# Performance work log

Measured on AMD Instinct MI355X. Metric: run time of the kernel, lower is better.

## Reference

```python
import jax, jax.numpy as jnp
import numpy as np

B, N, F, E, K, R, H = 16, 2048, 2048, 128, 10, 2, 2


def setup_inputs() -> dict:
    key = jax.random.key(0)
    ks = jax.random.split(key, 11)
    s = 0.1  # keep embeddings close so the Gaussian kernel does not underflow
    rel = jax.random.normal(ks[0], (B, E), jnp.float32) * s
    arg1 = jax.random.normal(ks[1], (B, E), jnp.float32) * s
    arg2 = jax.random.normal(ks[2], (B, E), jnp.float32) * s
    fact_rel = jax.random.normal(ks[3], (B, F, E), jnp.float32) * s
    fact_arg1 = jax.random.normal(ks[4], (B, F, E), jnp.float32) * s
    fact_arg2 = jax.random.normal(ks[5], (B, F, E), jnp.float32) * s
    entity_embeddings = jax.random.normal(ks[6], (B, N, E), jnp.float32) * s
    hop_W = jax.random.normal(ks[7], (R, H, E, E), jnp.float32) / jnp.sqrt(jnp.float32(E))
    hop_b = jax.random.normal(ks[8], (R, H, E), jnp.float32) * 0.01
    nb_facts = jax.random.randint(ks[9], (B,), F // 2, F + 1, jnp.int32)
    nb_entities = jax.random.randint(ks[10], (B,), N // 2, N + 1, jnp.int32)
    return dict(rel=rel, arg1=arg1, arg2=arg2, fact_rel=fact_rel,
                fact_arg1=fact_arg1, fact_arg2=fact_arg2,
                entity_embeddings=entity_embeddings, hop_W=hop_W, hop_b=hop_b,
                nb_facts=nb_facts, nb_entities=nb_entities)


def reference(rel, arg1, arg2, fact_rel, fact_arg1, fact_arg2,
              entity_embeddings, hop_W, hop_b, nb_facts, nb_entities):
    # Gaussian kernel k(x,y) = exp(-||x-y||^2 / 2), batched: x [B,T,E], y [B,F,E] -> [B,T,F]
    def kern(x, y):
        d2 = (jnp.sum(x * x, -1)[:, :, None] + jnp.sum(y * y, -1)[:, None, :]
              - 2.0 * jnp.einsum('bte,bfe->btf', x, y))
        return jnp.exp(-0.5 * d2)

    fact_mask = (jnp.arange(F) < nb_facts[:, None])[:, None, :]            # [B,1,F]
    ent_mask = (jnp.arange(N) < nb_entities[:, None]).astype(rel.dtype)    # [B,N]

    # BatchNeuralKB.score: max over (valid) facts of product of kernels. [B,T,E]x3 -> [B,T]
    def model_score(r, a1, a2):
        s = kern(r, fact_rel) * kern(a1, fact_arg1) * kern(a2, fact_arg2)  # [B,T,F]
        return jnp.max(jnp.where(fact_mask, s, 0.0), axis=-1)

    # BatchNeuralKB.forward, (s,p,?) -> score per candidate object entity. [B,1,E] -> [B,N]
    def forward_sp(r, a1):
        kr = jnp.where(fact_mask, kern(r, fact_rel) * kern(a1, fact_arg1), 0.0)  # [B,1,F]
        kE = kern(entity_embeddings, fact_arg2)                                  # [B,N,F]
        return jnp.max(kr * kE, axis=-1) * ent_mask                              # [B,N]

    # (?,p,o) -> score per candidate subject entity
    def forward_po(r, a2):
        kr = jnp.where(fact_mask, kern(r, fact_rel) * kern(a2, fact_arg2), 0.0)
        kE = kern(entity_embeddings, fact_arg1)
        return jnp.max(kr * kE, axis=-1) * ent_mask

    # r_score(depth=1) = max(depth_r_score(0), depth_r_score(1))
    # depth_r_score(0) == model.score
    scores_0 = model_score(rel[:, None], arg1[:, None], arg2[:, None])[:, 0]  # [B]

    global_res = None
    for r_idx in range(R):
        is_rev = (r_idx % 2 == 1)
        # LinearReformulator: hop relations from rel
        h1 = rel @ hop_W[r_idx, 0] + hop_b[r_idx, 0]  # [B,E]
        h2 = rel @ hop_W[r_idx, 1] + hop_b[r_idx, 1]
        # hop 1: r_hop -> scores over all entities, then top-k beam
        if is_rev:
            sp = forward_po(h1[:, None], arg1[:, None])  # [B,N]
        else:
            sp = forward_sp(h1[:, None], arg1[:, None])
        z_scores, z_idx = jax.lax.top_k(sp, K)                                  # [B,K]
        z_emb = jnp.take_along_axis(entity_embeddings, z_idx[:, :, None], axis=1)  # [B,K,E]
        # final hop: r_score(depth=0) == model.score with branched args
        h2k = jnp.broadcast_to(h2[:, None, :], (B, K, E))
        a2k = jnp.broadcast_to(arg2[:, None, :], (B, K, E))
        if is_rev:
            s2 = model_score(h2k, a2k, z_emb)  # [B,K]
        else:
            s2 = model_score(h2k, z_emb, a2k)
        rule_scores = jnp.minimum(s2, z_scores)   # tnorm = 'min'
        rule_res = jnp.max(rule_scores, axis=1)   # max over branches [B]
        global_res = rule_res if global_res is None else jnp.maximum(global_res, rule_res)

    return jnp.maximum(scores_0, global_res)
```

## Files before the change

### kernel.cpp

```cpp
#include <hip/hip_runtime.h>
#include <math.h>

#define Bb 16
#define Nn 2048
#define Ff 2048
#define Ee 128
#define Kk 10
#define S2FC 8
#define S2F (Ff / S2FC)

typedef __attribute__((ext_vector_type(8))) short short8;
typedef __attribute__((ext_vector_type(4))) float f32x4;

__device__ inline float wave_sum(float x) {
    for (int o = 32; o; o >>= 1) x += __shfl_down(x, o);
    return x;
}

__device__ inline void bsplit(float x, unsigned short& h, unsigned short& l) {
    unsigned int u = __float_as_uint(x);
    h = (unsigned short)(u >> 16);
    float hf = __uint_as_float(u & 0xFFFF0000u);
    l = (unsigned short)(__float_as_uint(x - hf) >> 16);
}

__global__ __launch_bounds__(256) void k_bsplit(
    const float* __restrict__ fa1, const float* __restrict__ fa2,
    unsigned short* __restrict__ B0, unsigned short* __restrict__ B1) {
    int tid = threadIdx.x;
    int oct = tid & 15, fl = tid >> 4;
    int bx = blockIdx.x;
    int b = bx >> 7, f = (bx & 127) * 16 + fl;
    const float* src = (blockIdx.y == 0) ? fa2 : fa1;
    unsigned short* dst = ((blockIdx.y == 0) ? B0 : B1) +
                          (((size_t)b * 16 + oct) * Ff + f) * 16;
    const float* s = src + ((size_t)b * Ff + f) * Ee + oct * 8;
    float4 v0 = *(const float4*)s;
    float4 v1 = *(const float4*)(s + 4);
    float xs[8] = {v0.x, v0.y, v0.z, v0.w, v1.x, v1.y, v1.z, v1.w};
    unsigned short hi[8], lo[8];
#pragma unroll
    for (int j = 0; j < 8; ++j) bsplit(xs[j], hi[j], lo[j]);
    uint4 ph, pl;
    ph.x = (unsigned)hi[0] | ((unsigned)hi[1] << 16);
    ph.y = (unsigned)hi[2] | ((unsigned)hi[3] << 16);
    ph.z = (unsigned)hi[4] | ((unsigned)hi[5] << 16);
    ph.w = (unsigned)hi[6] | ((unsigned)hi[7] << 16);
    pl.x = (unsigned)lo[0] | ((unsigned)lo[1] << 16);
    pl.y = (unsigned)lo[2] | ((unsigned)lo[3] << 16);
    pl.z = (unsigned)lo[4] | ((unsigned)lo[5] << 16);
    pl.w = (unsigned)lo[6] | ((unsigned)lo[7] << 16);
    *(uint4*)dst = ph;
    *(uint4*)(dst + 8) = pl;
}

__global__ void k_hops(const float* __restrict__ rel, const float* __restrict__ hop_W,
                       const float* __restrict__ hop_b, float* __restrict__ h) {
    int rj = blockIdx.x;
    int b  = blockIdx.y;
    int e  = threadIdx.x;
    const float* W  = hop_W + (size_t)rj * Ee * Ee;
    const float* rb = rel + b * Ee;
    float acc = hop_b[rj * Ee + e];
    for (int i = 0; i < Ee; ++i) acc += rb[i] * W[i * Ee + e];
    h[((size_t)rj * Bb + b) * Ee + e] = acc;
}

__global__ void k_entnorm(const float* __restrict__ ent, float* __restrict__ ent_norm) {
    int row  = blockIdx.x * 4 + (threadIdx.x >> 6);
    int lane = threadIdx.x & 63;
    const float* p = ent + (size_t)row * Ee;
    float a = p[lane], c = p[lane + 64];
    float s = wave_sum(a * a + c * c);
    if (lane == 0) ent_norm[row] = s;
}

__global__ void k_facts(const float* __restrict__ rel, const float* __restrict__ arg1,
                        const float* __restrict__ arg2, const float* __restrict__ frel,
                        const float* __restrict__ fa1, const float* __restrict__ fa2,
                        const float* __restrict__ h, const int* __restrict__ nb_facts,
                        float* __restrict__ c0, float* __restrict__ c1,
                        float* __restrict__ s2b0, float* __restrict__ s2b1,
                        float* __restrict__ lsc0) {
    int f = blockIdx.x, b = blockIdx.y;
    int lane = threadIdx.x;
    size_t fb = ((size_t)b * Ff + f) * Ee;
    float d_rr = 0, d_a11 = 0, d_a22 = 0, d_h10 = 0, d_h11 = 0, d_h20 = 0, d_h21 = 0;
    float d_a12 = 0, d_a21 = 0, n1 = 0, n2 = 0;
#pragma unroll
    for (int half = 0; half < 2; ++half) {
        int e = lane + half * 64;
        float vr = frel[fb + e], v1 = fa1[fb + e], v2 = fa2[fb + e];
        float qr = rel[b * Ee + e], q1 = arg1[b * Ee + e], q2 = arg2[b * Ee + e];
        float h10 = h[((size_t)0 * Bb + b) * Ee + e];
        float h20 = h[((size_t)1 * Bb + b) * Ee + e];
        float h11 = h[((size_t)2 * Bb + b) * Ee + e];
        float h21 = h[((size_t)3 * Bb + b) * Ee + e];
        float t;
        t = qr - vr;  d_rr  += t * t;
        t = q1 - v1;  d_a11 += t * t;
        t = q2 - v2;  d_a22 += t * t;
        t = h10 - vr; d_h10 += t * t;
        t = h11 - vr; d_h11 += t * t;
        t = h20 - vr; d_h20 += t * t;
        t = h21 - vr; d_h21 += t * t;
        t = q1 - v2;  d_a12 += t * t;
        t = q2 - v1;  d_a21 += t * t;
        n1 += v1 * v1; n2 += v2 * v2;
    }
    d_rr = wave_sum(d_rr);   d_a11 = wave_sum(d_a11); d_a22 = wave_sum(d_a22);
    d_h10 = wave_sum(d_h10); d_h11 = wave_sum(d_h11); d_h20 = wave_sum(d_h20);
    d_h21 = wave_sum(d_h21); d_a12 = wave_sum(d_a12); d_a21 = wave_sum(d_a21);
    n1 = wave_sum(n1);       n2 = wave_sum(n2);
    if (lane == 0) {
        bool valid = f < nb_facts[b];
        const float NI = -INFINITY;
        size_t o = (size_t)b * Ff + f;
        lsc0[o] = valid ? -0.5f * (d_rr + d_a11 + d_a22) : NI;
        c0[o]   = valid ? (-0.5f * (d_h10 + d_a11 + n2)) : NI;
        c1[o]   = valid ? (-0.5f * (d_h11 + d_a12 + n1)) : NI;
        s2b0[o] = valid ? (-0.5f * (d_h20 + d_a22)) : NI;
        s2b1[o] = valid ? (-0.5f * (d_h21 + d_a21)) : NI;
    }
}

#define BMs 128

__global__ __launch_bounds__(256, 2) void k_spmax_mfma(
    const float* __restrict__ ent, const unsigned short* __restrict__ B0,
    const unsigned short* __restrict__ B1, const float* __restrict__ c0,
    const float* __restrict__ c1, const float* __restrict__ ent_norm,
    const int* __restrict__ nb_entities, float* __restrict__ sp0,
    float* __restrict__ sp1) {
    int nblk = blockIdx.x, b = blockIdx.y, r = blockIdx.z;
    const unsigned short* Bt = (r == 0) ? B0 : B1;
    const float* cb = ((r == 0) ? c0 : c1) + (size_t)b * Ff;
    float* sp = ((r == 0) ? sp0 : sp1) + (size_t)b * Nn;

    __shared__ unsigned short alds[2 * 4 * 4 * 64 * 8];

    int tid = threadIdx.x;
    int wave = tid >> 6, lane = tid & 63;
    int wm = wave >> 1, wn = wave & 1;
    int lane15 = lane & 15, quad = lane >> 4;

    short8 ah[4][4];
    {
        const float* abase = ent + ((size_t)b * Nn + (size_t)nblk * BMs + wm * 64) * Ee;
#pragma unroll
        for (int i = 0; i < 4; ++i)
#pragma unroll
            for (int ks = 0; ks < 4; ++ks) {
                const float* p = abase + (size_t)(i * 16 + lane15) * Ee + ks * 32 + quad * 8;
                float4 v0 = *(const float4*)p;
                float4 v1 = *(const float4*)(p + 4);
                float xs[8] = {v0.x, v0.y, v0.z, v0.w, v1.x, v1.y, v1.z, v1.w};
                short8 hi8, lo8;
#pragma unroll
                for (int j = 0; j < 8; ++j) {
                    unsigned short hh, ll;
                    bsplit(xs[j], hh, ll);
                    hi8[j] = (short)hh;
                    lo8[j] = (short)ll;
                }
                ah[i][ks] = hi8;
                if (wn == 0)
                    *(short8*)&alds[(((wm * 4 + i) * 4 + ks) * 64 + lane) * 8] = lo8;
            }
    }
    __syncthreads();

    const unsigned short* bbase =
        Bt + ((((size_t)b * 16 + quad) * Ff) + wn * 32 + lane15) * 16;

    short8 pbh0[4], pbl0[4], pbh1[4], pbl1[4];
#pragma unroll
    for (int ks = 0; ks < 4; ++ks) {
        const unsigned short* p0 = bbase + ((size_t)ks * 4 * Ff) * 16;
        pbh0[ks] = *(const short8*)p0;
        pbl0[ks] = *(const short8*)(p0 + 8);
        pbh1[ks] = *(const short8*)(p0 + 256);
        pbl1[ks] = *(const short8*)(p0 + 264);
    }

    float mmax[4][4];
#pragma unroll
    for (int i = 0; i < 4; ++i)
#pragma unroll
        for (int rr = 0; rr < 4; ++rr) mmax[i][rr] = -INFINITY;

    for (int c = 0; c < 32; ++c) {
        int f0 = c * 64;
        float cj0 = cb[f0 + wn * 32 + lane15];
        float cj1 = cb[f0 + wn * 32 + 16 + lane15];
        f32x4 acc[4][2];
#pragma unroll
        for (int i = 0; i < 4; ++i) {
            acc[i][0] = (f32x4){cj0, cj0, cj0, cj0};
            acc[i][1] = (f32x4){cj1, cj1, cj1, cj1};
        }
        int fn = ((c + 1) & 31) * 64;

#pragma unroll
        for (int ks = 0; ks < 4; ++ks) {
            short8 bh0 = pbh0[ks], bl0 = pbl0[ks], bh1 = pbh1[ks], bl1 = pbl1[ks];
            const unsigned short* p0 = bbase + ((size_t)ks * 4 * Ff + fn) * 16;
            pbh0[ks] = *(const short8*)p0;
            pbl0[ks] = *(const short8*)(p0 + 8);
            pbh1[ks] = *(const short8*)(p0 + 256);
            pbl1[ks] = *(const short8*)(p0 + 264);
            short8 al0 = *(short8*)&alds[(((wm * 4 + 0) * 4 + ks) * 64 + lane) * 8];
            short8 al1 = *(short8*)&alds[(((wm * 4 + 1) * 4 + ks) * 64 + lane) * 8];
            short8 al2 = *(short8*)&alds[(((wm * 4 + 2) * 4 + ks) * 64 + lane) * 8];
            short8 al3 = *(short8*)&alds[(((wm * 4 + 3) * 4 + ks) * 64 + lane) * 8];
            short8 alv[4] = {al0, al1, al2, al3};
#pragma unroll
            for (int i = 0; i < 4; ++i) {
                acc[i][0] = __builtin_amdgcn_mfma_f32_16x16x32_bf16(ah[i][ks], bh0, acc[i][0], 0, 0, 0);
                acc[i][0] = __builtin_amdgcn_mfma_f32_16x16x32_bf16(alv[i],    bh0, acc[i][0], 0, 0, 0);
                acc[i][0] = __builtin_amdgcn_mfma_f32_16x16x32_bf16(ah[i][ks], bl0, acc[i][0], 0, 0, 0);
                acc[i][1] = __builtin_amdgcn_mfma_f32_16x16x32_bf16(ah[i][ks], bh1, acc[i][1], 0, 0, 0);
                acc[i][1] = __builtin_amdgcn_mfma_f32_16x16x32_bf16(alv[i],    bh1, acc[i][1], 0, 0, 0);
                acc[i][1] = __builtin_amdgcn_mfma_f32_16x16x32_bf16(ah[i][ks], bl1, acc[i][1], 0, 0, 0);
            }
        }

#pragma unroll
        for (int j = 0; j < 2; ++j)
#pragma unroll
            for (int i = 0; i < 4; ++i)
#pragma unroll
                for (int rr = 0; rr < 4; ++rr)
                    mmax[i][rr] = fmaxf(mmax[i][rr], acc[i][j][rr]);
    }

    __syncthreads();
    float* red = (float*)alds;
#pragma unroll
    for (int i = 0; i < 4; ++i)
#pragma unroll
        for (int rr = 0; rr < 4; ++rr) {
            float v = mmax[i][rr];
#pragma unroll
            for (int m = 1; m < 16; m <<= 1) v = fmaxf(v, __shfl_xor(v, m));
            if (lane15 == 0) red[(wm * 64 + i * 16 + quad * 4 + rr) * 2 + wn] = v;
        }
    __syncthreads();
    if (tid < BMs) {
        float m = fmaxf(red[tid * 2], red[tid * 2 + 1]);
        int n = nblk * BMs + tid;
        float v = (n < nb_entities[b]) ? expf(m - 0.5f * ent_norm[(size_t)b * Nn + n]) : 0.0f;
        sp[n] = v;
    }
}

__global__ void k_topk(const float* __restrict__ sp0, const float* __restrict__ sp1,
                       float* __restrict__ z_scores, int* __restrict__ z_idx) {
    int b = blockIdx.x, r = blockIdx.y;
    const float* sp = ((r == 0) ? sp0 : sp1) + (size_t)b * Nn;
    int lane = threadIdx.x;
    float v[Nn / 64];
#pragma unroll
    for (int i = 0; i < Nn / 64; ++i) v[i] = sp[i * 64 + lane];
    for (int k = 0; k < Kk; ++k) {
        float best = -INFINITY; int bidx = 0;
#pragma unroll
        for (int i = 0; i < Nn / 64; ++i)
            if (v[i] > best) { best = v[i]; bidx = i * 64 + lane; }
#pragma unroll
        for (int m = 1; m < 64; m <<= 1) {
            float ov = __shfl_xor(best, m);
            int oi = __shfl_xor(bidx, m);
            if (ov > best || (ov == best && oi < bidx)) { best = ov; bidx = oi; }
        }
        if (lane == 0) {
            z_scores[((size_t)b * 2 + r) * Kk + k] = best;
            z_idx[((size_t)b * 2 + r) * Kk + k]    = bidx;
        }
        if ((bidx & 63) == lane) {
            int slot = bidx >> 6;
#pragma unroll
            for (int i = 0; i < Nn / 64; ++i)
                if (i == slot) v[i] = -INFINITY;
        }
    }
}

__global__ __launch_bounds__(256) void k_s2(
    const float* __restrict__ ent, const float* __restrict__ fa1,
    const float* __restrict__ fa2, const float* __restrict__ s2b0,
    const float* __restrict__ s2b1, const int* __restrict__ z_idx,
    float* __restrict__ partial ) {
    int fc = blockIdx.x, b = blockIdx.y, r = blockIdx.z;
    const float* factX = (r == 0) ? fa1 : fa2;
    const float* s2b   = ((r == 0) ? s2b0 : s2b1) + (size_t)b * Ff;

    __shared__ float zsh[Kk][Ee];
    __shared__ float znorm[Kk];
    __shared__ int   zish[Kk];
    __shared__ float red[4][Kk];

    int tid = threadIdx.x;
    if (tid < Kk) zish[tid] = z_idx[((size_t)b * 2 + r) * Kk + tid];
    __syncthreads();
    for (int idx = tid; idx < Kk * Ee; idx += 256) {
        int k = idx >> 7, e = idx & 127;
        zsh[k][e] = ent[((size_t)b * Nn + zish[k]) * Ee + e];
    }
    __syncthreads();
    if (tid < Kk) {
        float s = 0.f;
        for (int e = 0; e < Ee; ++e) { float v = zsh[tid][e]; s += v * v; }
        znorm[tid] = s;
    }
    __syncthreads();

    int f = fc * S2F + tid;
    const float* fp = factX + ((size_t)b * Ff + f) * Ee;
    float acc[Kk];
#pragma unroll
    for (int k = 0; k < Kk; ++k) acc[k] = 0.f;
    float nf = 0.f;
#pragma unroll 4
    for (int e0 = 0; e0 < Ee; e0 += 4) {
        float4 v = *(const float4*)(fp + e0);
        nf += v.x * v.x + v.y * v.y + v.z * v.z + v.w * v.w;
#pragma unroll
        for (int k = 0; k < Kk; ++k) {
            float4 z = *(const float4*)&zsh[k][e0];
            acc[k] += z.x * v.x + z.y * v.y + z.z * v.z + z.w * v.w;
        }
    }
    float base = s2b[f] - 0.5f * nf;
    float sc[Kk];
#pragma unroll
    for (int k = 0; k < Kk; ++k) sc[k] = base + acc[k] - 0.5f * znorm[k];
    for (int o = 32; o; o >>= 1)
#pragma unroll
        for (int k = 0; k < Kk; ++k) sc[k] = fmaxf(sc[k], __shfl_down(sc[k], o));
    int wv = tid >> 6;
    if ((tid & 63) == 0)
#pragma unroll
        for (int k = 0; k < Kk; ++k) red[wv][k] = sc[k];
    __syncthreads();
    if (tid < Kk) {
        float m = fmaxf(fmaxf(red[0][tid], red[1][tid]), fmaxf(red[2][tid], red[3][tid]));
        partial[(((size_t)b * 2 + r) * S2FC + fc) * Kk + tid] = m;
    }
}

__global__ void k_final(const float* __restrict__ lsc0, const float* __restrict__ partial,
                        const float* __restrict__ z_scores, float* __restrict__ out) {
    int b = blockIdx.x, tid = threadIdx.x;
    __shared__ float sm[256];
    float m = -INFINITY;
    for (int f = tid; f < Ff; f += 256) m = fmaxf(m, lsc0[(size_t)b * Ff + f]);
    sm[tid] = m;
    __syncthreads();
    for (int s = 128; s > 0; s >>= 1) {
        if (tid < s) sm[tid] = fmaxf(sm[tid], sm[tid + s]);
        __syncthreads();
    }
    if (tid == 0) {
        float sc0 = expf(sm[0]);
        float g = -INFINITY;
        for (int r = 0; r < 2; ++r)
            for (int k = 0; k < Kk; ++k) {
                float mm = -INFINITY;
                for (int fc = 0; fc < S2FC; ++fc)
                    mm = fmaxf(mm, partial[(((size_t)b * 2 + r) * S2FC + fc) * Kk + k]);
                float rule = fminf(expf(mm), z_scores[((size_t)b * 2 + r) * Kk + k]);
                g = fmaxf(g, rule);
            }
        out[b] = fmaxf(sc0, g);
    }
}

extern "C" void kernel_launch(void* const* d_in, const int* in_sizes, int n_in,
                              void* d_out, int out_size, void* d_ws, size_t ws_size,
                              hipStream_t stream) {
    const float* rel  = (const float*)d_in[0];
    const float* arg1 = (const float*)d_in[1];
    const float* arg2 = (const float*)d_in[2];
    const float* frel = (const float*)d_in[3];
    const float* fa1  = (const float*)d_in[4];
    const float* fa2  = (const float*)d_in[5];
    const float* ent  = (const float*)d_in[6];
    const float* hopW = (const float*)d_in[7];
    const float* hopb = (const float*)d_in[8];
    const int* nb_facts    = (const int*)d_in[9];
    const int* nb_entities = (const int*)d_in[10];
    float* out = (float*)d_out;

    float* ws = (float*)d_ws;
    size_t off = 0;
    float* h        = ws + off; off += 4 * Bb * Ee;
    float* c0       = ws + off; off += (size_t)Bb * Ff;
    float* c1       = ws + off; off += (size_t)Bb * Ff;
    float* s2b0     = ws + off; off += (size_t)Bb * Ff;
    float* s2b1     = ws + off; off += (size_t)Bb * Ff;
    float* lsc0     = ws + off; off += (size_t)Bb * Ff;
    float* sp0      = ws + off; off += (size_t)Bb * Nn;
    float* sp1      = ws + off; off += (size_t)Bb * Nn;
    float* ent_norm = ws + off; off += (size_t)Bb * Nn;
    float* z_scores = ws + off; off += Bb * 2 * Kk;
    float* partial  = ws + off; off += (size_t)Bb * 2 * S2FC * Kk;
    int*   z_idx    = (int*)(ws + off); off += Bb * 2 * Kk;
    off = (off + 7) & ~(size_t)7;
    unsigned short* B0 = (unsigned short*)(ws + off); off += (size_t)Bb * 16 * Ff * 8;
    unsigned short* B1 = (unsigned short*)(ws + off); off += (size_t)Bb * 16 * Ff * 8;

    k_bsplit<<<dim3(Bb * Ff / 16, 2), 256, 0, stream>>>(fa1, fa2, B0, B1);
    k_hops<<<dim3(4, Bb), 128, 0, stream>>>(rel, hopW, hopb, h);
    k_entnorm<<<dim3(Bb * Nn / 4), 256, 0, stream>>>(ent, ent_norm);
    k_facts<<<dim3(Ff, Bb), 64, 0, stream>>>(rel, arg1, arg2, frel, fa1, fa2, h,
                                             nb_facts, c0, c1, s2b0, s2b1, lsc0);
    k_spmax_mfma<<<dim3(Nn / BMs, Bb, 2), 256, 0, stream>>>(ent, B0, B1, c0, c1, ent_norm,
                                                            nb_entities, sp0, sp1);
    k_topk<<<dim3(Bb, 2), 64, 0, stream>>>(sp0, sp1, z_scores, z_idx);
    k_s2<<<dim3(S2FC, Bb, 2), 256, 0, stream>>>(ent, fa1, fa2, s2b0, s2b1, z_idx, partial);
    k_final<<<dim3(Bb), 256, 0, stream>>>(lsc0, partial, z_scores, out);
}
```

Before: 264.3 us.

## Fuse prep, norm, top-k and final kernels; use atomic max output

```diff
diff --git a/kernel.cpp b/kernel.cpp
--- a/kernel.cpp
+++ b/kernel.cpp
@@ -24,55 +24,53 @@
     l = (unsigned short)(__float_as_uint(x - hf) >> 16);
 }
 
-__global__ __launch_bounds__(256) void k_bsplit(
-    const float* __restrict__ fa1, const float* __restrict__ fa2,
-    unsigned short* __restrict__ B0, unsigned short* __restrict__ B1) {
+__device__ inline void atomic_fmax_pos(float* addr, float v) {
+    atomicMax((unsigned int*)addr, __float_as_uint(v));
+}
+
+__global__ __launch_bounds__(256) void k_prep(
+    const float* __restrict__ rel, const float* __restrict__ hop_W,
+    const float* __restrict__ hop_b, const float* __restrict__ fa1,
+    const float* __restrict__ fa2, unsigned short* __restrict__ B0,
+    unsigned short* __restrict__ B1, float* __restrict__ h) {
+    int bx = blockIdx.x;
     int tid = threadIdx.x;
-    int oct = tid & 15, fl = tid >> 4;
-    int bx = blockIdx.x;
-    int b = bx >> 7, f = (bx & 127) * 16 + fl;
-    const float* src = (blockIdx.y == 0) ? fa2 : fa1;
-    unsigned short* dst = ((blockIdx.y == 0) ? B0 : B1) +
-                          (((size_t)b * 16 + oct) * Ff + f) * 16;
-    const float* s = src + ((size_t)b * Ff + f) * Ee + oct * 8;
-    float4 v0 = *(const float4*)s;
-    float4 v1 = *(const float4*)(s + 4);
-    float xs[8] = {v0.x, v0.y, v0.z, v0.w, v1.x, v1.y, v1.z, v1.w};
-    unsigned short hi[8], lo[8];
-#pragma unroll
-    for (int j = 0; j < 8; ++j) bsplit(xs[j], hi[j], lo[j]);
-    uint4 ph, pl;
-    ph.x = (unsigned)hi[0] | ((unsigned)hi[1] << 16);
-    ph.y = (unsigned)hi[2] | ((unsigned)hi[3] << 16);
-    ph.z = (unsigned)hi[4] | ((unsigned)hi[5] << 16);
-    ph.w = (unsigned)hi[6] | ((unsigned)hi[7] << 16);
-    pl.x = (unsigned)lo[0] | ((unsigned)lo[1] << 16);
-    pl.y = (unsigned)lo[2] | ((unsigned)lo[3] << 16);
-    pl.z = (unsigned)lo[4] | ((unsigned)lo[5] << 16);
-    pl.w = (unsigned)lo[6] | ((unsigned)lo[7] << 16);
-    *(uint4*)dst = ph;
-    *(uint4*)(dst + 8) = pl;
-}
-
-__global__ void k_hops(const float* __restrict__ rel, const float* __restrict__ hop_W,
-                       const float* __restrict__ hop_b, float* __restrict__ h) {
-    int rj = blockIdx.x;
-    int b  = blockIdx.y;
-    int e  = threadIdx.x;
-    const float* W  = hop_W + (size_t)rj * Ee * Ee;
-    const float* rb = rel + b * Ee;
-    float acc = hop_b[rj * Ee + e];
-    for (int i = 0; i < Ee; ++i) acc += rb[i] * W[i * Ee + e];
-    h[((size_t)rj * Bb + b) * Ee + e] = acc;
-}
-
-__global__ void k_entnorm(const float* __restrict__ ent, float* __restrict__ ent_norm) {
-    int row  = blockIdx.x * 4 + (threadIdx.x >> 6);
-    int lane = threadIdx.x & 63;
-    const float* p = ent + (size_t)row * Ee;
-    float a = p[lane], c = p[lane + 64];
-    float s = wave_sum(a * a + c * c);
-    if (lane == 0) ent_norm[row] = s;
+    if (bx < 4096) {
+        int y = bx >> 11, bxi = bx & 2047;
+        int oct = tid & 15, fl = tid >> 4;
+        int b = bxi >> 7, f = (bxi & 127) * 16 + fl;
+        const float* src = (y == 0) ? fa2 : fa1;
+        unsigned short* dst = ((y == 0) ? B0 : B1) +
+                              (((size_t)b * 16 + oct) * Ff + f) * 16;
+        const float* s = src + ((size_t)b * Ff + f) * Ee + oct * 8;
+        float4 v0 = *(const float4*)s;
+        float4 v1 = *(const float4*)(s + 4);
+        float xs[8] = {v0.x, v0.y, v0.z, v0.w, v1.x, v1.y, v1.z, v1.w};
+        unsigned short hi[8], lo[8];
+#pragma unroll
+        for (int j = 0; j < 8; ++j) bsplit(xs[j], hi[j], lo[j]);
+        uint4 ph, pl;
+        ph.x = (unsigned)hi[0] | ((unsigned)hi[1] << 16);
+        ph.y = (unsigned)hi[2] | ((unsigned)hi[3] << 16);
+        ph.z = (unsigned)hi[4] | ((unsigned)hi[5] << 16);
+        ph.w = (unsigned)hi[6] | ((unsigned)hi[7] << 16);
+        pl.x = (unsigned)lo[0] | ((unsigned)lo[1] << 16);
+        pl.y = (unsigned)lo[2] | ((unsigned)lo[3] << 16);
+        pl.z = (unsigned)lo[4] | ((unsigned)lo[5] << 16);
+        pl.w = (unsigned)lo[6] | ((unsigned)lo[7] << 16);
+        *(uint4*)dst = ph;
+        *(uint4*)(dst + 8) = pl;
+    } else {
+        int idx = (bx - 4096) * 256 + tid;
+        int rj = idx >> 11;
+        int b  = (idx >> 7) & 15;
+        int e  = idx & 127;
+        const float* W  = hop_W + (size_t)rj * Ee * Ee;
+        const float* rb = rel + b * Ee;
+        float acc = hop_b[rj * Ee + e];
+        for (int q = 0; q < Ee; ++q) acc += rb[q] * W[q * Ee + e];
+        h[((size_t)rj * Bb + b) * Ee + e] = acc;
+    }
 }
 
 __global__ void k_facts(const float* __restrict__ rel, const float* __restrict__ arg1,
@@ -81,7 +79,7 @@
                         const float* __restrict__ h, const int* __restrict__ nb_facts,
                         float* __restrict__ c0, float* __restrict__ c1,
                         float* __restrict__ s2b0, float* __restrict__ s2b1,
-                        float* __restrict__ lsc0) {
+                        float* __restrict__ out) {
     int f = blockIdx.x, b = blockIdx.y;
     int lane = threadIdx.x;
     size_t fb = ((size_t)b * Ff + f) * Ee;
@@ -116,11 +114,12 @@
         bool valid = f < nb_facts[b];
         const float NI = -INFINITY;
         size_t o = (size_t)b * Ff + f;
-        lsc0[o] = valid ? -0.5f * (d_rr + d_a11 + d_a22) : NI;
         c0[o]   = valid ? (-0.5f * (d_h10 + d_a11 + n2)) : NI;
         c1[o]   = valid ? (-0.5f * (d_h11 + d_a12 + n1)) : NI;
         s2b0[o] = valid ? (-0.5f * (d_h20 + d_a22)) : NI;
         s2b1[o] = valid ? (-0.5f * (d_h21 + d_a21)) : NI;
+        float lsc = valid ? (-0.5f * (d_rr + d_a11 + d_a22)) : NI;
+        atomic_fmax_pos(out + b, expf(lsc));
     }
 }
 
@@ -129,15 +128,17 @@
 __global__ __launch_bounds__(256, 2) void k_spmax_mfma(
     const float* __restrict__ ent, const unsigned short* __restrict__ B0,
     const unsigned short* __restrict__ B1, const float* __restrict__ c0,
-    const float* __restrict__ c1, const float* __restrict__ ent_norm,
-    const int* __restrict__ nb_entities, float* __restrict__ sp0,
-    float* __restrict__ sp1) {
-    int nblk = blockIdx.x, b = blockIdx.y, r = blockIdx.z;
+    const float* __restrict__ c1, const int* __restrict__ nb_entities,
+    float* __restrict__ sp0, float* __restrict__ sp1) {
+    int bid = blockIdx.x;
+    int br = bid & 31, nblk = bid >> 5;
+    int b = br >> 1, r = br & 1;
     const unsigned short* Bt = (r == 0) ? B0 : B1;
     const float* cb = ((r == 0) ? c0 : c1) + (size_t)b * Ff;
     float* sp = ((r == 0) ? sp0 : sp1) + (size_t)b * Nn;
 
     __shared__ unsigned short alds[2 * 4 * 4 * 64 * 8];
+    __shared__ float normsh[BMs];
 
     int tid = threadIdx.x;
     int wave = tid >> 6, lane = tid & 63;
@@ -148,7 +149,8 @@
     {
         const float* abase = ent + ((size_t)b * Nn + (size_t)nblk * BMs + wm * 64) * Ee;
 #pragma unroll
-        for (int i = 0; i < 4; ++i)
+        for (int i = 0; i < 4; ++i) {
+            float sq = 0.f;
 #pragma unroll
             for (int ks = 0; ks < 4; ++ks) {
                 const float* p = abase + (size_t)(i * 16 + lane15) * Ee + ks * 32 + quad * 8;
@@ -162,11 +164,17 @@
                     bsplit(xs[j], hh, ll);
                     hi8[j] = (short)hh;
                     lo8[j] = (short)ll;
+                    sq += xs[j] * xs[j];
                 }
                 ah[i][ks] = hi8;
                 if (wn == 0)
                     *(short8*)&alds[(((wm * 4 + i) * 4 + ks) * 64 + lane) * 8] = lo8;
             }
+            float v = sq;
+            v += __shfl_xor(v, 16);
+            v += __shfl_xor(v, 32);
+            if (wn == 0 && quad == 0) normsh[wm * 64 + i * 16 + lane15] = v;
+        }
     }
     __syncthreads();
 
@@ -182,6 +190,10 @@
         pbh1[ks] = *(const short8*)(p0 + 256);
         pbl1[ks] = *(const short8*)(p0 + 264);
     }
+    short8 bufA[4], bufB[4];
+#pragma unroll
+    for (int i = 0; i < 4; ++i)
+        bufA[i] = *(short8*)&alds[(((wm * 4 + i) * 4 + 0) * 64 + lane) * 8];
 
     float mmax[4][4];
 #pragma unroll
@@ -209,18 +221,19 @@
             pbl0[ks] = *(const short8*)(p0 + 8);
             pbh1[ks] = *(const short8*)(p0 + 256);
             pbl1[ks] = *(const short8*)(p0 + 264);
-            short8 al0 = *(short8*)&alds[(((wm * 4 + 0) * 4 + ks) * 64 + lane) * 8];
-            short8 al1 = *(short8*)&alds[(((wm * 4 + 1) * 4 + ks) * 64 + lane) * 8];
-            short8 al2 = *(short8*)&alds[(((wm * 4 + 2) * 4 + ks) * 64 + lane) * 8];
-            short8 al3 = *(short8*)&alds[(((wm * 4 + 3) * 4 + ks) * 64 + lane) * 8];
-            short8 alv[4] = {al0, al1, al2, al3};
+            short8* cur = (ks & 1) ? bufB : bufA;
+            short8* nxt = (ks & 1) ? bufA : bufB;
+            int nks = (ks + 1) & 3;
+#pragma unroll
+            for (int i = 0; i < 4; ++i)
+                nxt[i] = *(short8*)&alds[(((wm * 4 + i) * 4 + nks) * 64 + lane) * 8];
 #pragma unroll
             for (int i = 0; i < 4; ++i) {
                 acc[i][0] = __builtin_amdgcn_mfma_f32_16x16x32_bf16(ah[i][ks], bh0, acc[i][0], 0, 0, 0);
-                acc[i][0] = __builtin_amdgcn_mfma_f32_16x16x32_bf16(alv[i],    bh0, acc[i][0], 0, 0, 0);
+                acc[i][0] = __builtin_amdgcn_mfma_f32_16x16x32_bf16(cur[i],    bh0, acc[i][0], 0, 0, 0);
                 acc[i][0] = __builtin_amdgcn_mfma_f32_16x16x32_bf16(ah[i][ks], bl0, acc[i][0], 0, 0, 0);
                 acc[i][1] = __builtin_amdgcn_mfma_f32_16x16x32_bf16(ah[i][ks], bh1, acc[i][1], 0, 0, 0);
-                acc[i][1] = __builtin_amdgcn_mfma_f32_16x16x32_bf16(alv[i],    bh1, acc[i][1], 0, 0, 0);
+                acc[i][1] = __builtin_amdgcn_mfma_f32_16x16x32_bf16(cur[i],    bh1, acc[i][1], 0, 0, 0);
                 acc[i][1] = __builtin_amdgcn_mfma_f32_16x16x32_bf16(ah[i][ks], bl1, acc[i][1], 0, 0, 0);
             }
         }
@@ -249,63 +262,58 @@
     if (tid < BMs) {
         float m = fmaxf(red[tid * 2], red[tid * 2 + 1]);
         int n = nblk * BMs + tid;
-        float v = (n < nb_entities[b]) ? expf(m - 0.5f * ent_norm[(size_t)b * Nn + n]) : 0.0f;
+        float v = (n < nb_entities[b]) ? expf(m - 0.5f * normsh[tid]) : 0.0f;
         sp[n] = v;
     }
 }
 
-__global__ void k_topk(const float* __restrict__ sp0, const float* __restrict__ sp1,
-                       float* __restrict__ z_scores, int* __restrict__ z_idx) {
-    int b = blockIdx.x, r = blockIdx.y;
-    const float* sp = ((r == 0) ? sp0 : sp1) + (size_t)b * Nn;
-    int lane = threadIdx.x;
-    float v[Nn / 64];
-#pragma unroll
-    for (int i = 0; i < Nn / 64; ++i) v[i] = sp[i * 64 + lane];
-    for (int k = 0; k < Kk; ++k) {
-        float best = -INFINITY; int bidx = 0;
-#pragma unroll
-        for (int i = 0; i < Nn / 64; ++i)
-            if (v[i] > best) { best = v[i]; bidx = i * 64 + lane; }
-#pragma unroll
-        for (int m = 1; m < 64; m <<= 1) {
-            float ov = __shfl_xor(best, m);
-            int oi = __shfl_xor(bidx, m);
-            if (ov > best || (ov == best && oi < bidx)) { best = ov; bidx = oi; }
-        }
-        if (lane == 0) {
-            z_scores[((size_t)b * 2 + r) * Kk + k] = best;
-            z_idx[((size_t)b * 2 + r) * Kk + k]    = bidx;
-        }
-        if ((bidx & 63) == lane) {
-            int slot = bidx >> 6;
-#pragma unroll
-            for (int i = 0; i < Nn / 64; ++i)
-                if (i == slot) v[i] = -INFINITY;
-        }
-    }
-}
-
-__global__ __launch_bounds__(256) void k_s2(
+__global__ __launch_bounds__(256) void k_s2t(
     const float* __restrict__ ent, const float* __restrict__ fa1,
     const float* __restrict__ fa2, const float* __restrict__ s2b0,
-    const float* __restrict__ s2b1, const int* __restrict__ z_idx,
-    float* __restrict__ partial ) {
+    const float* __restrict__ s2b1, const float* __restrict__ sp0,
+    const float* __restrict__ sp1, float* __restrict__ out) {
     int fc = blockIdx.x, b = blockIdx.y, r = blockIdx.z;
     const float* factX = (r == 0) ? fa1 : fa2;
     const float* s2b   = ((r == 0) ? s2b0 : s2b1) + (size_t)b * Ff;
-
+    const float* sp    = ((r == 0) ? sp0 : sp1) + (size_t)b * Nn;
+
+    __shared__ float zsc[Kk];
+    __shared__ int   zidx[Kk];
     __shared__ float zsh[Kk][Ee];
     __shared__ float znorm[Kk];
-    __shared__ int   zish[Kk];
     __shared__ float red[4][Kk];
 
     int tid = threadIdx.x;
-    if (tid < Kk) zish[tid] = z_idx[((size_t)b * 2 + r) * Kk + tid];
+    int wv = tid >> 6, lane = tid & 63;
+
+    if (wv == 0) {
+        float v[Nn / 64];
+#pragma unroll
+        for (int i = 0; i < Nn / 64; ++i) v[i] = sp[i * 64 + lane];
+        for (int k = 0; k < Kk; ++k) {
+            float best = -INFINITY; int bidx = 0;
+#pragma unroll
+            for (int i = 0; i < Nn / 64; ++i)
+                if (v[i] > best) { best = v[i]; bidx = i * 64 + lane; }
+#pragma unroll
+            for (int m = 1; m < 64; m <<= 1) {
+                float ov = __shfl_xor(best, m);
+                int oi = __shfl_xor(bidx, m);
+                if (ov > best || (ov == best && oi < bidx)) { best = ov; bidx = oi; }
+            }
+            if (lane == 0) { zsc[k] = best; zidx[k] = bidx; }
+            if ((bidx & 63) == lane) {
+                int slot = bidx >> 6;
+#pragma unroll
+                for (int i = 0; i < Nn / 64; ++i)
+                    if (i == slot) v[i] = -INFINITY;
+            }
+        }
+    }
     __syncthreads();
     for (int idx = tid; idx < Kk * Ee; idx += 256) {
         int k = idx >> 7, e = idx & 127;
-        zsh[k][e] = ent[((size_t)b * Nn + zish[k]) * Ee + e];
+        zsh[k][e] = ent[((size_t)b * Nn + zidx[k]) * Ee + e];
     }
     __syncthreads();
     if (tid < Kk) {
@@ -338,41 +346,13 @@
     for (int o = 32; o; o >>= 1)
 #pragma unroll
         for (int k = 0; k < Kk; ++k) sc[k] = fmaxf(sc[k], __shfl_down(sc[k], o));
-    int wv = tid >> 6;
     if ((tid & 63) == 0)
 #pragma unroll
         for (int k = 0; k < Kk; ++k) red[wv][k] = sc[k];
     __syncthreads();
     if (tid < Kk) {
         float m = fmaxf(fmaxf(red[0][tid], red[1][tid]), fmaxf(red[2][tid], red[3][tid]));
-        partial[(((size_t)b * 2 + r) * S2FC + fc) * Kk + tid] = m;
-    }
-}
-
-__global__ void k_final(const float* __restrict__ lsc0, const float* __restrict__ partial,
-                        const float* __restrict__ z_scores, float* __restrict__ out) {
-    int b = blockIdx.x, tid = threadIdx.x;
-    __shared__ float sm[256];
-    float m = -INFINITY;
-    for (int f = tid; f < Ff; f += 256) m = fmaxf(m, lsc0[(size_t)b * Ff + f]);
-    sm[tid] = m;
-    __syncthreads();
-    for (int s = 128; s > 0; s >>= 1) {
-        if (tid < s) sm[tid] = fmaxf(sm[tid], sm[tid + s]);
-        __syncthreads();
-    }
-    if (tid == 0) {
-        float sc0 = expf(sm[0]);
-        float g = -INFINITY;
-        for (int r = 0; r < 2; ++r)
-            for (int k = 0; k < Kk; ++k) {
-                float mm = -INFINITY;
-                for (int fc = 0; fc < S2FC; ++fc)
-                    mm = fmaxf(mm, partial[(((size_t)b * 2 + r) * S2FC + fc) * Kk + k]);
-                float rule = fminf(expf(mm), z_scores[((size_t)b * 2 + r) * Kk + k]);
-                g = fmaxf(g, rule);
-            }
-        out[b] = fmaxf(sc0, g);
+        atomic_fmax_pos(out + b, fminf(expf(m), zsc[tid]));
     }
 }
 
@@ -399,25 +379,18 @@
     float* c1       = ws + off; off += (size_t)Bb * Ff;
     float* s2b0     = ws + off; off += (size_t)Bb * Ff;
     float* s2b1     = ws + off; off += (size_t)Bb * Ff;
-    float* lsc0     = ws + off; off += (size_t)Bb * Ff;
     float* sp0      = ws + off; off += (size_t)Bb * Nn;
     float* sp1      = ws + off; off += (size_t)Bb * Nn;
-    float* ent_norm = ws + off; off += (size_t)Bb * Nn;
-    float* z_scores = ws + off; off += Bb * 2 * Kk;
-    float* partial  = ws + off; off += (size_t)Bb * 2 * S2FC * Kk;
-    int*   z_idx    = (int*)(ws + off); off += Bb * 2 * Kk;
     off = (off + 7) & ~(size_t)7;
     unsigned short* B0 = (unsigned short*)(ws + off); off += (size_t)Bb * 16 * Ff * 8;
     unsigned short* B1 = (unsigned short*)(ws + off); off += (size_t)Bb * 16 * Ff * 8;
 
-    k_bsplit<<<dim3(Bb * Ff / 16, 2), 256, 0, stream>>>(fa1, fa2, B0, B1);
-    k_hops<<<dim3(4, Bb), 128, 0, stream>>>(rel, hopW, hopb, h);
-    k_entnorm<<<dim3(Bb * Nn / 4), 256, 0, stream>>>(ent, ent_norm);
+    hipMemsetAsync(d_out, 0, (size_t)out_size * sizeof(float), stream);
+    k_prep<<<dim3(4096 + 32), 256, 0, stream>>>(rel, hopW, hopb, fa1, fa2, B0, B1, h);
     k_facts<<<dim3(Ff, Bb), 64, 0, stream>>>(rel, arg1, arg2, frel, fa1, fa2, h,
-                                             nb_facts, c0, c1, s2b0, s2b1, lsc0);
-    k_spmax_mfma<<<dim3(Nn / BMs, Bb, 2), 256, 0, stream>>>(ent, B0, B1, c0, c1, ent_norm,
-                                                            nb_entities, sp0, sp1);
-    k_topk<<<dim3(Bb, 2), 64, 0, stream>>>(sp0, sp1, z_scores, z_idx);
-    k_s2<<<dim3(S2FC, Bb, 2), 256, 0, stream>>>(ent, fa1, fa2, s2b0, s2b1, z_idx, partial);
-    k_final<<<dim3(Bb), 256, 0, stream>>>(lsc0, partial, z_scores, out);
-}
+                                             nb_facts, c0, c1, s2b0, s2b1, out);
+    k_spmax_mfma<<<dim3(512), 256, 0, stream>>>(ent, B0, B1, c0, c1,
+                                                nb_entities, sp0, sp1);
+    k_s2t<<<dim3(S2FC, Bb, 2), 256, 0, stream>>>(ent, fa1, fa2, s2b0, s2b1,
+                                                 sp0, sp1, out);
+}
```

After: 611.3 us. 131% more time.
